# Kernel tuning notes

Measured on AMD Instinct MI355X. Metric: run time of the kernel, lower is better.

The kernel has to match this reference:

```python
import jax, jax.numpy as jnp
import numpy as np

TEMPERATURE = 8.0   # sqrt(d_k), d_k = 64
TOP_K = 5           # SparseAttention default top_k in mimicry/RIMs
EPS = 1e-7          # matches torch 10e-8


def _sparsify(attn_rows):
    """Per-row top-k sparsification: keep mass above the k-th largest value,
    clamp at zero, renormalize. attn_rows: [N, L]."""
    topk_vals = jax.lax.top_k(attn_rows, TOP_K)[0]          # [N, K]
    delta = topk_vals[:, -1:] + EPS                          # k-th largest per row
    w = jnp.maximum(attn_rows - delta, 0.0)                  # clamp(min=0)
    return w / (jnp.sum(w, axis=1, keepdims=True) + EPS)


def setup_inputs() -> dict:
    key = jax.random.key(0)
    kq, kk, kv = jax.random.split(key, 3)
    B, L, D = 4, 4096, 64
    q = jax.random.normal(kq, (B, L, D), dtype=jnp.float32)
    k = jax.random.normal(kk, (B, L, D), dtype=jnp.float32)
    v = jax.random.normal(kv, (B, L, D), dtype=jnp.float32)
    return {"q": q, "k": k, "v": v}


def reference(q, k, v):
    # attn = softmax(q k^T / temperature); dropout is identity in eval mode
    attn = jnp.einsum('bqd,bkd->bqk', q / TEMPERATURE, k)   # [B, Lq, Lk]
    attn = jax.nn.softmax(attn, axis=-1)
    B, Lq, Lk = attn.shape
    attn = _sparsify(attn.reshape(B * Lq, Lk)).reshape(B, Lq, Lk)
    out = jnp.einsum('bqk,bkd->bqd', attn, v)               # [B, Lq, Dv]
    return out, attn
```

## Files before the change

kernel.cpp:

```cpp
#include <hip/hip_runtime.h>
#include <math.h>

#define NB 4
#define L 4096
#define D 64
#define WS_QL 1048576
#define WS_K  2097152
#define KBS   524288
#define KPL   262144
#define QSCALE 0.1803368801111243f

typedef __attribute__((ext_vector_type(8))) short short8;
typedef __attribute__((ext_vector_type(4))) float floatx4;

static __device__ inline ushort2 f2bf2(float x) {
    unsigned int u = __builtin_bit_cast(unsigned int, x);
    unsigned int uh = u + (0x7FFFu + ((u >> 16) & 1u));
    unsigned short h = (unsigned short)(uh >> 16);
    float hf = __builtin_bit_cast(float, (unsigned int)h << 16);
    float r = x - hf;
    unsigned int v = __builtin_bit_cast(unsigned int, r);
    unsigned short l = (unsigned short)((v + (0x7FFFu + ((v >> 16) & 1u))) >> 16);
    ushort2 p; p.x = h; p.y = l; return p;
}

__global__ __launch_bounds__(256)
void convert_kernel(const float* __restrict__ qg, const float* __restrict__ kg,
                    unsigned short* __restrict__ ws) {
    unsigned int i = blockIdx.x * 256 + threadIdx.x;
    if (i < 262144) {
        float4 qv = ((const float4*)qg)[i];
        ushort2 p0 = f2bf2(qv.x * QSCALE), p1 = f2bf2(qv.y * QSCALE),
                p2 = f2bf2(qv.z * QSCALE), p3 = f2bf2(qv.w * QSCALE);
        ushort4 h; h.x = p0.x; h.y = p1.x; h.z = p2.x; h.w = p3.x;
        ushort4 l; l.x = p0.y; l.y = p1.y; l.z = p2.y; l.w = p3.y;
        *(ushort4*)&ws[i * 4] = h;
        *(ushort4*)&ws[WS_QL + i * 4] = l;
    } else {
        unsigned int j = i - 262144;
        float4 kv = ((const float4*)kg)[j];
        ushort2 p0 = f2bf2(kv.x), p1 = f2bf2(kv.y), p2 = f2bf2(kv.z), p3 = f2bf2(kv.w);
        ushort4 h; h.x = p0.x; h.y = p1.x; h.z = p2.x; h.w = p3.x;
        ushort4 l; l.x = p0.y; l.y = p1.y; l.z = p2.y; l.w = p3.y;
        unsigned int bcol = j >> 4;
        unsigned int f4   = j & 15;
        unsigned int b    = bcol >> 12, col = bcol & 4095;
        unsigned int cq   = f4 >> 1, half = f4 & 1;
        size_t base = WS_K + (size_t)b * KBS + ((size_t)cq * 4096 + col) * 8 + half * 4;
        *(ushort4*)&ws[base] = h;
        *(ushort4*)&ws[base + KPL] = l;
    }
}

static __device__ inline void ins5(float d[5], float t) {
    float n0 = fmaxf(d[0], t);
    float n1 = __builtin_amdgcn_fmed3f(t, d[0], d[1]);
    float n2 = __builtin_amdgcn_fmed3f(t, d[1], d[2]);
    float n3 = __builtin_amdgcn_fmed3f(t, d[2], d[3]);
    float n4 = __builtin_amdgcn_fmed3f(t, d[3], d[4]);
    d[0] = n0; d[1] = n1; d[2] = n2; d[3] = n3; d[4] = n4;
}

static __device__ inline void merge5(float d[5], const float o[5]) {
#pragma unroll
    for (int j = 0; j < 5; ++j) {
        float t = o[j];
        float carry = d[j];
        d[j] = fmaxf(d[j], t);
#pragma unroll
        for (int k = j + 1; k < 5; ++k) {
            float pk = d[k];
            d[k] = __builtin_amdgcn_fmed3f(t, carry, d[k]);
            carry = pk;
        }
    }
}

__global__ __launch_bounds__(512, 4)
void sparse_attn_kernel(const unsigned short* __restrict__ ws,
                        const float* __restrict__ vg,
                        float* __restrict__ outg) {
    __shared__ float smv[2][4][16][5];

    const int tid  = threadIdx.x;
    const int lane = tid & 63;
    const int wid  = tid >> 6;
    const int cq   = wid & 3;
    const int rh   = wid >> 2;
    const int c16  = lane & 15;
    const int quad = lane >> 4;

    const int sblk  = (blockIdx.x & 7) * 64 + (blockIdx.x >> 3);
    const int qbase = sblk * 32;
    const int qbw   = qbase + rh * 16;
    const int b     = qbase >> 12;
    const int phase = sblk & 63;

    const unsigned short* qh   = ws;
    const unsigned short* ql   = ws + WS_QL;
    const unsigned short* kbat = ws + WS_K + (size_t)b * KBS;
    const float* vb = vg + (size_t)b * L * D;
    float* attng = outg + (size_t)NB * L * D;

    const int qrow = qbw + c16;
    const short8 a0h = *(const short8*)&qh[(size_t)qrow * 64 + quad * 8];
    const short8 a1h = *(const short8*)&qh[(size_t)qrow * 64 + 32 + quad * 8];
    const short8 a0l = *(const short8*)&ql[(size_t)qrow * 64 + quad * 8];
    const short8 a1l = *(const short8*)&ql[(size_t)qrow * 64 + 32 + quad * 8];

    float tv[5];
#pragma unroll
    for (int i = 0; i < 5; ++i) tv[i] = -INFINITY;

    const int colq = cq * 1024;
    const unsigned short* bp0 = kbat + ((size_t)(quad)     * 4096 + colq + c16) * 8;
    const unsigned short* bp1 = kbat + ((size_t)(4 + quad) * 4096 + colq + c16) * 8;
    const float4 zv = make_float4(0.f, 0.f, 0.f, 0.f);

    const int colb0 = colq + quad * 4;

#pragma unroll 4
    for (int cg0 = 0; cg0 < 64; ++cg0) {
        int cg = cg0 + phase;
        cg = (cg >= 64) ? cg - 64 : cg;

        const int off = cg * 128;
        short8 b0h = *(const short8*)(bp0 + off);
        short8 b1h = *(const short8*)(bp1 + off);
        short8 b0l = *(const short8*)(bp0 + KPL + off);
        short8 b1l = *(const short8*)(bp1 + KPL + off);
        floatx4 acc = {0.f, 0.f, 0.f, 0.f};
        acc = __builtin_amdgcn_mfma_f32_16x16x32_bf16(b0h, a0h, acc, 0, 0, 0);
        acc = __builtin_amdgcn_mfma_f32_16x16x32_bf16(b1h, a1h, acc, 0, 0, 0);
        acc = __builtin_amdgcn_mfma_f32_16x16x32_bf16(b0h, a0l, acc, 0, 0, 0);
        acc = __builtin_amdgcn_mfma_f32_16x16x32_bf16(b1h, a1l, acc, 0, 0, 0);
        acc = __builtin_amdgcn_mfma_f32_16x16x32_bf16(b0l, a0h, acc, 0, 0, 0);
        acc = __builtin_amdgcn_mfma_f32_16x16x32_bf16(b1l, a1h, acc, 0, 0, 0);

        {
            int idx = cg * 64 + lane;
            *(float4*)&attng[(size_t)(qbw + (idx >> 8)) * L + colq + (idx & 255) * 4] = zv;
        }

        const int cxb = (colb0 + cg * 16) ^ 4095;
#pragma unroll
        for (int r = 0; r < 4; ++r) {
            int si  = __builtin_bit_cast(int, (float)acc[r]);
            int tag = (cxb ^ r) ^ ((si >> 31) & 4095);
            int ti  = (si & 0xFFFFF000) | tag;
            ins5(tv, __builtin_bit_cast(float, ti));
        }
    }

#pragma unroll
    for (int m = 16; m <= 32; m <<= 1) {
        float o[5];
#pragma unroll
        for (int i = 0; i < 5; ++i) o[i] = __shfl_xor(tv[i], m, 64);
        merge5(tv, o);
    }

    if (quad == 0) {
#pragma unroll
        for (int i = 0; i < 5; ++i) smv[rh][cq][c16][i] = tv[i];
    }
    __syncthreads();

    if (cq == 0) {
#pragma unroll
        for (int r = 0; r < 4; ++r) {
            const int rowl = quad * 4 + r;
            float lv[5];
#pragma unroll
            for (int i = 0; i < 5; ++i) lv[i] = smv[rh][0][rowl][i];
#pragma unroll
            for (int f = 1; f < 4; ++f) {
                float o[5];
#pragma unroll
                for (int i = 0; i < 5; ++i) o[i] = smv[rh][f][rowl][i];
                merge5(lv, o);
            }

            int t0 = __builtin_bit_cast(int, lv[0]);
            int t1 = __builtin_bit_cast(int, lv[1]);
            int t2 = __builtin_bit_cast(int, lv[2]);
            int t3 = __builtin_bit_cast(int, lv[3]);
            unsigned int i0 = (unsigned)((t0 & 4095) ^ (t0 >= 0 ? 4095 : 0));
            unsigned int i1 = (unsigned)((t1 & 4095) ^ (t1 >= 0 ? 4095 : 0));
            unsigned int i2 = (unsigned)((t2 & 4095) ^ (t2 >= 0 ? 4095 : 0));
            unsigned int i3 = (unsigned)((t3 & 4095) ^ (t3 >= 0 ? 4095 : 0));

            float u0 = exp2f(lv[0] - lv[4]) - 1.0f;
            float u1 = exp2f(lv[1] - lv[4]) - 1.0f;
            float u2 = exp2f(lv[2] - lv[4]) - 1.0f;
            float u3 = exp2f(lv[3] - lv[4]) - 1.0f;
            float inv = 1.0f / (u0 + u1 + u2 + u3 + 1e-30f);
            float w0 = u0 * inv, w1 = u1 * inv, w2 = u2 * inv, w3 = u3 * inv;

            const int rowabs = qbw + rowl;

            const float4 v0 = *(const float4*)(vb + (size_t)i0 * D + c16 * 4);
            const float4 v1 = *(const float4*)(vb + (size_t)i1 * D + c16 * 4);
            const float4 v2 = *(const float4*)(vb + (size_t)i2 * D + c16 * 4);
            const float4 v3 = *(const float4*)(vb + (size_t)i3 * D + c16 * 4);
            float4 o;
            o.x = w0 * v0.x + w1 * v1.x + w2 * v2.x + w3 * v3.x;
            o.y = w0 * v0.y + w1 * v1.y + w2 * v2.y + w3 * v3.y;
            o.z = w0 * v0.z + w1 * v1.z + w2 * v2.z + w3 * v3.z;
            o.w = w0 * v0.w + w1 * v1.w + w2 * v2.w + w3 * v3.w;
            *(float4*)(outg + (size_t)rowabs * D + c16 * 4) = o;

            if (c16 < 4) {
                float wv = c16 == 0 ? w0 : c16 == 1 ? w1 : c16 == 2 ? w2 : w3;
                unsigned int cs = c16 == 0 ? i0 : c16 == 1 ? i1
                                : c16 == 2 ? i2 : i3;
                if (wv > 0.f)
                    attng[(size_t)rowabs * L + cs] = wv;
            }
        }
    }
}

extern "C" void kernel_launch(void* const* d_in, const int* in_sizes, int n_in,
                              void* d_out, int out_size, void* d_ws, size_t ws_size,
                              hipStream_t stream) {
    const float* q = (const float*)d_in[0];
    const float* k = (const float*)d_in[1];
    const float* v = (const float*)d_in[2];
    float* out = (float*)d_out;
    unsigned short* ws = (unsigned short*)d_ws;

    convert_kernel<<<2048, 256, 0, stream>>>(q, k, ws);

    sparse_attn_kernel<<<512, 512, 0, stream>>>(ws, v, out);
}
```

Before: 303.0 us.

## Use single-bf16 QK screening with top-8 candidates and exact fp32 rescoring

Replaces the split hi/lo bf16 three-pass product (six MFMAs per tile) with a single bf16 pass (two MFMAs) and halves the K/Q workspace traffic. To recover accuracy it keeps top-8 candidates per row instead of top-5, then recomputes exact fp32 dot products for those 8 from the original q and k, sorts them and picks the top-5. This cuts MFMA work and global loads in the main loop. In exchange it adds longer insertion and merge chains, more registers, and a small gather-and-shuffle rescoring step, and it risks mis-ranking when the true top-5 falls outside the bf16 top-8.

```diff
diff --git a/kernel.cpp b/kernel.cpp
--- a/kernel.cpp
+++ b/kernel.cpp
@@ -4,24 +4,16 @@
 #define NB 4
 #define L 4096
 #define D 64
-#define WS_QL 1048576
-#define WS_K  2097152
-#define KBS   524288
-#define KPL   262144
+#define WS_K  1048576
+#define KBS   262144
 #define QSCALE 0.1803368801111243f
 
 typedef __attribute__((ext_vector_type(8))) short short8;
 typedef __attribute__((ext_vector_type(4))) float floatx4;
 
-static __device__ inline ushort2 f2bf2(float x) {
+static __device__ inline unsigned short f2bf(float x) {
     unsigned int u = __builtin_bit_cast(unsigned int, x);
-    unsigned int uh = u + (0x7FFFu + ((u >> 16) & 1u));
-    unsigned short h = (unsigned short)(uh >> 16);
-    float hf = __builtin_bit_cast(float, (unsigned int)h << 16);
-    float r = x - hf;
-    unsigned int v = __builtin_bit_cast(unsigned int, r);
-    unsigned short l = (unsigned short)((v + (0x7FFFu + ((v >> 16) & 1u))) >> 16);
-    ushort2 p; p.x = h; p.y = l; return p;
+    return (unsigned short)((u + (0x7FFFu + ((u >> 16) & 1u))) >> 16);
 }
 
 __global__ __launch_bounds__(256)
@@ -30,45 +22,45 @@
     unsigned int i = blockIdx.x * 256 + threadIdx.x;
     if (i < 262144) {
         float4 qv = ((const float4*)qg)[i];
-        ushort2 p0 = f2bf2(qv.x * QSCALE), p1 = f2bf2(qv.y * QSCALE),
-                p2 = f2bf2(qv.z * QSCALE), p3 = f2bf2(qv.w * QSCALE);
-        ushort4 h; h.x = p0.x; h.y = p1.x; h.z = p2.x; h.w = p3.x;
-        ushort4 l; l.x = p0.y; l.y = p1.y; l.z = p2.y; l.w = p3.y;
+        ushort4 h;
+        h.x = f2bf(qv.x * QSCALE); h.y = f2bf(qv.y * QSCALE);
+        h.z = f2bf(qv.z * QSCALE); h.w = f2bf(qv.w * QSCALE);
         *(ushort4*)&ws[i * 4] = h;
-        *(ushort4*)&ws[WS_QL + i * 4] = l;
     } else {
         unsigned int j = i - 262144;
         float4 kv = ((const float4*)kg)[j];
-        ushort2 p0 = f2bf2(kv.x), p1 = f2bf2(kv.y), p2 = f2bf2(kv.z), p3 = f2bf2(kv.w);
-        ushort4 h; h.x = p0.x; h.y = p1.x; h.z = p2.x; h.w = p3.x;
-        ushort4 l; l.x = p0.y; l.y = p1.y; l.z = p2.y; l.w = p3.y;
+        ushort4 h;
+        h.x = f2bf(kv.x); h.y = f2bf(kv.y); h.z = f2bf(kv.z); h.w = f2bf(kv.w);
         unsigned int bcol = j >> 4;
         unsigned int f4   = j & 15;
         unsigned int b    = bcol >> 12, col = bcol & 4095;
         unsigned int cq   = f4 >> 1, half = f4 & 1;
         size_t base = WS_K + (size_t)b * KBS + ((size_t)cq * 4096 + col) * 8 + half * 4;
         *(ushort4*)&ws[base] = h;
-        *(ushort4*)&ws[base + KPL] = l;
-    }
-}
-
-static __device__ inline void ins5(float d[5], float t) {
+    }
+}
+
+static __device__ inline void ins8(float d[8], float t) {
     float n0 = fmaxf(d[0], t);
     float n1 = __builtin_amdgcn_fmed3f(t, d[0], d[1]);
     float n2 = __builtin_amdgcn_fmed3f(t, d[1], d[2]);
     float n3 = __builtin_amdgcn_fmed3f(t, d[2], d[3]);
     float n4 = __builtin_amdgcn_fmed3f(t, d[3], d[4]);
-    d[0] = n0; d[1] = n1; d[2] = n2; d[3] = n3; d[4] = n4;
-}
-
-static __device__ inline void merge5(float d[5], const float o[5]) {
-#pragma unroll
-    for (int j = 0; j < 5; ++j) {
+    float n5 = __builtin_amdgcn_fmed3f(t, d[4], d[5]);
+    float n6 = __builtin_amdgcn_fmed3f(t, d[5], d[6]);
+    float n7 = __builtin_amdgcn_fmed3f(t, d[6], d[7]);
+    d[0] = n0; d[1] = n1; d[2] = n2; d[3] = n3;
+    d[4] = n4; d[5] = n5; d[6] = n6; d[7] = n7;
+}
+
+static __device__ inline void merge8(float d[8], const float o[8]) {
+#pragma unroll
+    for (int j = 0; j < 8; ++j) {
         float t = o[j];
         float carry = d[j];
         d[j] = fmaxf(d[j], t);
 #pragma unroll
-        for (int k = j + 1; k < 5; ++k) {
+        for (int k = j + 1; k < 8; ++k) {
             float pk = d[k];
             d[k] = __builtin_amdgcn_fmed3f(t, carry, d[k]);
             carry = pk;
@@ -78,9 +70,11 @@
 
 __global__ __launch_bounds__(512, 4)
 void sparse_attn_kernel(const unsigned short* __restrict__ ws,
+                        const float* __restrict__ qg,
+                        const float* __restrict__ kg,
                         const float* __restrict__ vg,
                         float* __restrict__ outg) {
-    __shared__ float smv[2][4][16][5];
+    __shared__ float smv[2][4][16][8];
 
     const int tid  = threadIdx.x;
     const int lane = tid & 63;
@@ -97,7 +91,6 @@
     const int phase = sblk & 63;
 
     const unsigned short* qh   = ws;
-    const unsigned short* ql   = ws + WS_QL;
     const unsigned short* kbat = ws + WS_K + (size_t)b * KBS;
     const float* vb = vg + (size_t)b * L * D;
     float* attng = outg + (size_t)NB * L * D;
@@ -105,12 +98,10 @@
     const int qrow = qbw + c16;
     const short8 a0h = *(const short8*)&qh[(size_t)qrow * 64 + quad * 8];
     const short8 a1h = *(const short8*)&qh[(size_t)qrow * 64 + 32 + quad * 8];
-    const short8 a0l = *(const short8*)&ql[(size_t)qrow * 64 + quad * 8];
-    const short8 a1l = *(const short8*)&ql[(size_t)qrow * 64 + 32 + quad * 8];
-
-    float tv[5];
-#pragma unroll
-    for (int i = 0; i < 5; ++i) tv[i] = -INFINITY;
+
+    float tv[8];
+#pragma unroll
+    for (int i = 0; i < 8; ++i) tv[i] = -INFINITY;
 
     const int colq = cq * 1024;
     const unsigned short* bp0 = kbat + ((size_t)(quad)     * 4096 + colq + c16) * 8;
@@ -127,15 +118,9 @@
         const int off = cg * 128;
         short8 b0h = *(const short8*)(bp0 + off);
         short8 b1h = *(const short8*)(bp1 + off);
-        short8 b0l = *(const short8*)(bp0 + KPL + off);
-        short8 b1l = *(const short8*)(bp1 + KPL + off);
         floatx4 acc = {0.f, 0.f, 0.f, 0.f};
         acc = __builtin_amdgcn_mfma_f32_16x16x32_bf16(b0h, a0h, acc, 0, 0, 0);
         acc = __builtin_amdgcn_mfma_f32_16x16x32_bf16(b1h, a1h, acc, 0, 0, 0);
-        acc = __builtin_amdgcn_mfma_f32_16x16x32_bf16(b0h, a0l, acc, 0, 0, 0);
-        acc = __builtin_amdgcn_mfma_f32_16x16x32_bf16(b1h, a1l, acc, 0, 0, 0);
-        acc = __builtin_amdgcn_mfma_f32_16x16x32_bf16(b0l, a0h, acc, 0, 0, 0);
-        acc = __builtin_amdgcn_mfma_f32_16x16x32_bf16(b1l, a1h, acc, 0, 0, 0);
 
         {
             int idx = cg * 64 + lane;
@@ -148,21 +133,21 @@
             int si  = __builtin_bit_cast(int, (float)acc[r]);
             int tag = (cxb ^ r) ^ ((si >> 31) & 4095);
             int ti  = (si & 0xFFFFF000) | tag;
-            ins5(tv, __builtin_bit_cast(float, ti));
+            ins8(tv, __builtin_bit_cast(float, ti));
         }
     }
 
 #pragma unroll
     for (int m = 16; m <= 32; m <<= 1) {
-        float o[5];
-#pragma unroll
-        for (int i = 0; i < 5; ++i) o[i] = __shfl_xor(tv[i], m, 64);
-        merge5(tv, o);
+        float o[8];
+#pragma unroll
+        for (int i = 0; i < 8; ++i) o[i] = __shfl_xor(tv[i], m, 64);
+        merge8(tv, o);
     }
 
     if (quad == 0) {
 #pragma unroll
-        for (int i = 0; i < 5; ++i) smv[rh][cq][c16][i] = tv[i];
+        for (int i = 0; i < 8; ++i) smv[rh][cq][c16][i] = tv[i];
     }
     __syncthreads();
 
@@ -170,39 +155,61 @@
 #pragma unroll
         for (int r = 0; r < 4; ++r) {
             const int rowl = quad * 4 + r;
-            float lv[5];
-#pragma unroll
-            for (int i = 0; i < 5; ++i) lv[i] = smv[rh][0][rowl][i];
+            float lv[8];
+#pragma unroll
+            for (int i = 0; i < 8; ++i) lv[i] = smv[rh][0][rowl][i];
 #pragma unroll
             for (int f = 1; f < 4; ++f) {
-                float o[5];
-#pragma unroll
-                for (int i = 0; i < 5; ++i) o[i] = smv[rh][f][rowl][i];
-                merge5(lv, o);
-            }
-
-            int t0 = __builtin_bit_cast(int, lv[0]);
-            int t1 = __builtin_bit_cast(int, lv[1]);
-            int t2 = __builtin_bit_cast(int, lv[2]);
-            int t3 = __builtin_bit_cast(int, lv[3]);
-            unsigned int i0 = (unsigned)((t0 & 4095) ^ (t0 >= 0 ? 4095 : 0));
-            unsigned int i1 = (unsigned)((t1 & 4095) ^ (t1 >= 0 ? 4095 : 0));
-            unsigned int i2 = (unsigned)((t2 & 4095) ^ (t2 >= 0 ? 4095 : 0));
-            unsigned int i3 = (unsigned)((t3 & 4095) ^ (t3 >= 0 ? 4095 : 0));
-
-            float u0 = exp2f(lv[0] - lv[4]) - 1.0f;
-            float u1 = exp2f(lv[1] - lv[4]) - 1.0f;
-            float u2 = exp2f(lv[2] - lv[4]) - 1.0f;
-            float u3 = exp2f(lv[3] - lv[4]) - 1.0f;
+                float o[8];
+#pragma unroll
+                for (int i = 0; i < 8; ++i) o[i] = smv[rh][f][rowl][i];
+                merge8(lv, o);
+            }
+
+            unsigned int ic[8];
+#pragma unroll
+            for (int j = 0; j < 8; ++j) {
+                int t = __builtin_bit_cast(int, lv[j]);
+                ic[j] = (unsigned)((t & 4095) ^ (t >= 0 ? 4095 : 0));
+            }
+
+            const int rowabs = qbw + rowl;
+
+            const float4 qv = *(const float4*)(qg + (size_t)rowabs * D + c16 * 4);
+            float s[8];
+#pragma unroll
+            for (int j = 0; j < 8; ++j) {
+                const float4 kv = *(const float4*)(kg + ((size_t)(b * L) + ic[j]) * D + c16 * 4);
+                float p = qv.x * kv.x + qv.y * kv.y + qv.z * kv.z + qv.w * kv.w;
+                p += __shfl_xor(p, 1, 64);
+                p += __shfl_xor(p, 2, 64);
+                p += __shfl_xor(p, 4, 64);
+                p += __shfl_xor(p, 8, 64);
+                s[j] = p * QSCALE;
+            }
+
+#pragma unroll
+            for (int j = 0; j < 5; ++j)
+#pragma unroll
+                for (int k = j + 1; k < 8; ++k) {
+                    bool sw = s[k] > s[j];
+                    float ts = sw ? s[k] : s[j];
+                    s[k] = sw ? s[j] : s[k];  s[j] = ts;
+                    unsigned int tc2 = sw ? ic[k] : ic[j];
+                    ic[k] = sw ? ic[j] : ic[k]; ic[j] = tc2;
+                }
+
+            float u0 = fmaxf(exp2f(s[0] - s[4]) - 1.0f, 0.0f);
+            float u1 = fmaxf(exp2f(s[1] - s[4]) - 1.0f, 0.0f);
+            float u2 = fmaxf(exp2f(s[2] - s[4]) - 1.0f, 0.0f);
+            float u3 = fmaxf(exp2f(s[3] - s[4]) - 1.0f, 0.0f);
             float inv = 1.0f / (u0 + u1 + u2 + u3 + 1e-30f);
             float w0 = u0 * inv, w1 = u1 * inv, w2 = u2 * inv, w3 = u3 * inv;
 
-            const int rowabs = qbw + rowl;
-
-            const float4 v0 = *(const float4*)(vb + (size_t)i0 * D + c16 * 4);
-            const float4 v1 = *(const float4*)(vb + (size_t)i1 * D + c16 * 4);
-            const float4 v2 = *(const float4*)(vb + (size_t)i2 * D + c16 * 4);
-            const float4 v3 = *(const float4*)(vb + (size_t)i3 * D + c16 * 4);
+            const float4 v0 = *(const float4*)(vb + (size_t)ic[0] * D + c16 * 4);
+            const float4 v1 = *(const float4*)(vb + (size_t)ic[1] * D + c16 * 4);
+            const float4 v2 = *(const float4*)(vb + (size_t)ic[2] * D + c16 * 4);
+            const float4 v3 = *(const float4*)(vb + (size_t)ic[3] * D + c16 * 4);
             float4 o;
             o.x = w0 * v0.x + w1 * v1.x + w2 * v2.x + w3 * v3.x;
             o.y = w0 * v0.y + w1 * v1.y + w2 * v2.y + w3 * v3.y;
@@ -212,8 +219,7 @@
 
             if (c16 < 4) {
                 float wv = c16 == 0 ? w0 : c16 == 1 ? w1 : c16 == 2 ? w2 : w3;
-                unsigned int cs = c16 == 0 ? i0 : c16 == 1 ? i1
-                                : c16 == 2 ? i2 : i3;
+                unsigned int cs = ic[c16];
                 if (wv > 0.f)
                     attng[(size_t)rowabs * L + cs] = wv;
             }
@@ -232,5 +238,5 @@
 
     convert_kernel<<<2048, 256, 0, stream>>>(q, k, ws);
 
-    sparse_attn_kernel<<<512, 512, 0, stream>>>(ws, v, out);
-}
+    sparse_attn_kernel<<<512, 512, 0, stream>>>(ws, q, k, v, out);
+}
```

Result: slower. 323.7 us (+6.8%).
